# Kernel tuning notes

Measured on AMD Instinct MI355X. Metric: run time of the kernel, lower is better.

The kernel has to match this reference:

```python
import jax, jax.numpy as jnp
import numpy as np

DECAY = 0.1  # decay_rate from init

def setup_inputs() -> dict:
    key = jax.random.key(0)
    ks = jax.random.split(key, 6)
    B, S, D, H = 64, 512, 256, 512
    x = jax.random.normal(ks[0], (B, S, D), dtype=jnp.float32)
    # layer 0: Linear(D+H, 4H); layer 1: Linear(H+H, 4H). Stored as [in, out].
    W0 = jax.random.normal(ks[1], (D + H, 4 * H), dtype=jnp.float32) * (1.0 / np.sqrt(D + H))
    b0 = jnp.zeros((4 * H,), dtype=jnp.float32)
    W1 = jax.random.normal(ks[2], (H + H, 4 * H), dtype=jnp.float32) * (1.0 / np.sqrt(H + H))
    b1 = jnp.zeros((4 * H,), dtype=jnp.float32)
    efw = jnp.zeros((1, 1, D), dtype=jnp.float32)  # nn.Parameter(torch.ones) would be ones; use small init via zeros->exp=1 equiv scale
    efw = jnp.ones((1, 1, D), dtype=jnp.float32)
    return {"x": x, "W0": W0, "b0": b0, "W1": W1, "b1": b1, "efw": efw}

def _cell(x_t, h_prev, c_prev, W, b):
    # combined: [B, in+H]; gates: [B, 4H] split into i,f,g,o along feature dim
    gates = jnp.concatenate([x_t, h_prev], axis=1) @ W + b
    i, f, g, o = jnp.split(gates, 4, axis=1)
    i = jax.nn.sigmoid(i)
    f = jax.nn.sigmoid(f + c_prev) * (1.0 - DECAY)  # custom decayed forget gate
    g = jnp.tanh(g)
    o = jax.nn.sigmoid(o)
    c_next = f * c_prev + i * g
    h_next = o * jnp.tanh(c_next)
    return h_next, c_next

def reference(x, W0, b0, W1, b1, efw):
    B, S, D = x.shape
    H = W0.shape[1] // 4
    x = x * jnp.exp(efw)  # elementwise feature weighting
    xs = jnp.transpose(x, (1, 0, 2))  # [S, B, D] for scan over time
    init = (jnp.zeros((B, H), x.dtype), jnp.zeros((B, H), x.dtype),
            jnp.zeros((B, H), x.dtype), jnp.zeros((B, H), x.dtype))

    def step(carry, x_t):
        h0, c0, h1, c1 = carry
        h0, c0 = _cell(x_t, h0, c0, W0, b0)
        h1, c1 = _cell(h0, h1, c1, W1, b1)
        return (h0, c0, h1, c1), h1

    _, ys = jax.lax.scan(step, init, xs)  # ys: [S, B, H]
    return jnp.transpose(ys, (1, 0, 2))  # [B, S, H]
```

## Files before the change

### kernel.cpp

```cpp
#include <hip/hip_runtime.h>
#include <math.h>

#define B_   64
#define S_   512
#define D_   256
#define H_   512
#define G4   2048
#define K0   768
#define K1   1024
#define NWG  256
#define NAH  128
#define NTHR 256
#define BH   32768
#define NROT 4

#define OFF_GF   32
#define OFF_SCL  192
#define OFF_FLG  512
#define OFF_EPO  4608
#define OFF_TKT  4736
#define OFF_ACN  4864
#define OFF_RLS  4992
#define OFF_XCN  5120
#define OFF_H0   5248
#define OFF_H1   (OFF_H0 + 2*BH)
#define OFF_C0   (OFF_H1 + 2*BH)
#define OFF_C1   (OFF_C0 + BH)
#define OFF_ZEND (OFF_C1 + BH)
#define OFF_XBUF OFF_ZEND
#define XBUF_SZ  (8 * NROT * 2 * BH)
#define OFF_END  (OFF_XBUF + XBUF_SZ)

typedef __attribute__((ext_vector_type(4))) float f32x4;
typedef __attribute__((ext_vector_type(8))) short s16x8;

__device__ __forceinline__ float sigm(float v){ return 1.0f/(1.0f+expf(-v)); }
__device__ __forceinline__ unsigned short f2bf(float f){
  unsigned u = __builtin_bit_cast(unsigned, f);
  return (unsigned short)((u + 0x7FFFu + ((u>>16)&1u)) >> 16);
}
__device__ __forceinline__ float bf2f(unsigned short s){
  return __builtin_bit_cast(float, ((unsigned)s) << 16);
}
__device__ __forceinline__ void split8(const float* v, s16x8& h, s16x8& l){
#pragma unroll
  for (int e = 0; e < 8; ++e){
    unsigned short hs = f2bf(v[e]);
    h[e] = (short)hs;
    l[e] = (short)f2bf(v[e] - bf2f(hs));
  }
}

#define ALD(p)   __hip_atomic_load((p), __ATOMIC_RELAXED, __HIP_MEMORY_SCOPE_AGENT)
#define AST(p,v) __hip_atomic_store((p), (v), __ATOMIC_RELAXED, __HIP_MEMORY_SCOPE_AGENT)

__device__ __forceinline__ void xadd_noret(unsigned* p, unsigned v){
  asm volatile("global_atomic_add %0, %1, off\n\ts_waitcnt vmcnt(0)"
               :: "v"(p), "v"(v) : "memory");
}
__device__ __forceinline__ unsigned xadd_ret0(unsigned* p){
  unsigned r, z = 0u;
  asm volatile("global_atomic_add %0, %1, %2, off sc0\n\ts_waitcnt vmcnt(0)"
               : "=&v"(r) : "v"(p), "v"(z) : "memory");
  return r;
}
__device__ __forceinline__ void ld2x4_sc1(const float* p, f32x4& a, f32x4& b){
  asm volatile("global_load_dwordx4 %0, %2, off sc1\n\t"
               "global_load_dwordx4 %1, %2, off offset:16 sc1\n\t"
               "s_waitcnt vmcnt(0)"
               : "=&v"(a), "=&v"(b) : "v"(p) : "memory");
}

__global__ void lstm_init(const float* __restrict__ efw, float* __restrict__ ws){
  int stride = gridDim.x * blockDim.x;
  for (int j = blockIdx.x * blockDim.x + threadIdx.x; j < OFF_ZEND; j += stride){
    float v = 0.0f;
    if (j >= OFF_SCL && j < OFF_SCL + D_) v = expf(efw[j - OFF_SCL]);
    ws[j] = v;
  }
}

__launch_bounds__(NTHR, 1)
__global__ void lstm_persist(const float* __restrict__ x,
                             const float* __restrict__ W0,
                             const float* __restrict__ b0,
                             const float* __restrict__ W1,
                             const float* __restrict__ b1,
                             float* __restrict__ out,
                             float* __restrict__ ws)
{
  __shared__ short wfH[32*64*8];
  __shared__ short wfL[32*64*8];
  __shared__ short afH[16*64*8];
  __shared__ short afL[16*64*8];
  __shared__ float zB[64*17];
  __shared__ float scl[D_];
  __shared__ int   sslot;

  const int  wg  = blockIdx.x;
  const int  tid = threadIdx.x;
  const bool isA = (wg < NAH);
  const int  u0  = (isA ? wg : wg - NAH) * 4;
  const int  KI  = isA ? 24 : 32;
  const int  nch = isA ? 6 : 8;
  const int  lane = tid & 63;
  const int  wv_  = tid >> 6;

  float* h0 = ws + OFF_H0;
  float* h1 = ws + OFF_H1;
  float* cs = ws + (isA ? OFF_C0 : OFF_C1);
  short* XB = (short*)(ws + OFF_XBUF);
  unsigned* gf  = (unsigned*)ws + OFF_GF;
  unsigned* epo = (unsigned*)ws + OFF_EPO;
  unsigned* flg = (unsigned*)ws + OFF_FLG;
  unsigned* tkt = (unsigned*)ws + OFF_TKT;

  {
    const float* W = isA ? W0 : W1;
    for (int f = tid; f < KI*64; f += NTHR){
      int ki = f >> 6, ln = f & 63;
      int col = ln & 15, g = col >> 2, u2 = col & 3;
      int kb = ki*32 + ((ln >> 4) << 3);
      const float* wp = W + (size_t)kb * G4 + g * H_ + u0 + u2;
      s16x8 hh, ll;
#pragma unroll
      for (int e = 0; e < 8; ++e){
        float w = wp[(size_t)e * G4];
        unsigned short hs = f2bf(w);
        hh[e] = (short)hs;
        ll[e] = (short)f2bf(w - bf2f(hs));
      }
      *(s16x8*)&wfH[(size_t)f * 8] = hh;
      *(s16x8*)&wfL[(size_t)f * 8] = ll;
    }
  }
  for (int i = tid; i < D_; i += NTHR) scl[i] = ws[OFF_SCL + i];

  int xcc, slot, nx = 1;
  {
    xcc = (int)(__builtin_amdgcn_s_getreg(63508) & 7u);
    if (tid == 0)
      sslot = (int)__hip_atomic_fetch_add(tkt + (size_t)xcc*16, 1u,
                 __ATOMIC_RELAXED, __HIP_MEMORY_SCOPE_AGENT);
    __syncthreads();
    slot = sslot;
  }
  unsigned* acnt = (unsigned*)ws + OFF_ACN + (size_t)xcc*16;
  unsigned* rls  = (unsigned*)ws + OFF_RLS + (size_t)xcc*16;
  unsigned* xcnt = (unsigned*)ws + OFF_XCN + (size_t)xcc*16;

  auto gbar = [&](unsigned tgt){
    __syncthreads();
    if (tid == 0) AST(flg + (size_t)wg * 16, tgt);
    if (wg == 0 && tid < 64){
      for (;;){
        unsigned m0 = ALD(flg + (size_t)(tid       ) * 16);
        unsigned m1 = ALD(flg + (size_t)(tid +  64) * 16);
        unsigned m2 = ALD(flg + (size_t)(tid + 128) * 16);
        unsigned m3 = ALD(flg + (size_t)(tid + 192) * 16);
        if (__all(m0 >= tgt && m1 >= tgt && m2 >= tgt && m3 >= tgt)) break;
      }
      if (tid == 0){
#pragma unroll
        for (int kq = 0; kq < 8; ++kq) AST(epo + (size_t)kq * 16, tgt);
      }
    }
    if (tid < 64){
      while (ALD(epo + (size_t)(wg & 7) * 16) < tgt)
        __builtin_amdgcn_s_sleep(4);
    }
    __syncthreads();
  };

  auto hbar = [&](unsigned ev){
    __syncthreads();
    if (tid == 0){
      xadd_noret(acnt, 1u);
      if (slot == 0){
        const unsigned tgt = ev * (unsigned)nx;
        while (xadd_ret0(acnt) < tgt) __builtin_amdgcn_s_sleep(2);
      }
    }
    if (slot == 0 && tid < 64){
      if (tid == 0) AST(gf + (size_t)xcc * 16, ev);
      unsigned v = ev;
      for (;;){
        if (tid < 8) v = ALD(gf + (size_t)tid * 16);
        if (__all(v >= ev)) break;
        __builtin_amdgcn_s_sleep(2);
      }
      if (tid == 0) xadd_noret(rls, 1u);
    }
    if (tid == 0){
      while (xadd_ret0(rls) < ev) __builtin_amdgcn_s_sleep(4);
    }
    __syncthreads();
  };

  auto xbar = [&](unsigned ev){
    __syncthreads();
    if (tid == 0){
      xadd_noret(xcnt, 1u);
      const unsigned tgt = ev * (unsigned)nx;
      while (xadd_ret0(xcnt) < tgt) __builtin_amdgcn_s_sleep(4);
    }
    __syncthreads();
  };

  gbar(1u);
  nx = (int)ALD(tkt + (size_t)xcc * 16);

  auto stage_xcd = [&](int q, int rot){
    short* sbw = XB + ((size_t)(xcc * NROT + rot)) * (4 * BH);
    for (int s = slot; s < 32; s += nx){
      int off = s * 2048 + tid * 8;
      const float* gs = (off < BH) ? ws + OFF_H0 + (size_t)q * BH + off
                                   : ws + OFF_H1 + (size_t)q * BH + (off - BH);
      f32x4 a, b; ld2x4_sc1(gs, a, b);
      float v[8] = {a[0], a[1], a[2], a[3], b[0], b[1], b[2], b[3]};
      s16x8 hh, ll; split8(v, hh, ll);
      *(s16x8*)(sbw + off)          = hh;
      *(s16x8*)(sbw + 2*BH + off)   = ll;
    }
  };

  stage_xcd(1, 3);
  xbar(1u);

  const int row_r = tid & 63;
  const int uu    = tid >> 6;
  float bias[4];
  {
    const float* bv = isA ? b0 : b1;
#pragma unroll
    for (int g = 0; g < 4; ++g) bias[g] = bv[g * H_ + u0 + uu];
  }
  __syncthreads();

  const short* sb = nullptr;
  s16x8 rh[4], rl[4];
  const int r16 = tid & 15, ksl = (tid >> 4) & 3, kiq = tid >> 6;

  auto loadregs = [&](int c, int t){
    const int kk = c * 128 + kiq * 32 + ksl * 8;
#pragma unroll
    for (int j = 0; j < 4; ++j){
      const int row = 16 * j + r16;
      if (isA && kk < 256){
        const float* xp = x + ((size_t)row * S_ + t) * D_ + kk;
        float4 v0 = *(const float4*)xp;
        float4 v1 = *(const float4*)(xp + 4);
        float4 s0 = *(const float4*)&scl[kk];
        float4 s1 = *(const float4*)&scl[kk + 4];
        float v[8] = {v0.x*s0.x, v0.y*s0.y, v0.z*s0.z, v0.w*s0.w,
                      v1.x*s1.x, v1.y*s1.y, v1.z*s1.z, v1.w*s1.w};
        split8(v, rh[j], rl[j]);
      } else {
        const short* hp;
        if (isA)           hp = sb + (size_t)row * H_ + (kk - 256);
        else if (kk < 512) hp = sb + (size_t)row * H_ + kk;
        else               hp = sb + BH + (size_t)row * H_ + (kk - 512);
        rh[j] = *(const s16x8*)hp;
        rl[j] = *(const s16x8*)(hp + 2 * BH);
      }
    }
  };

  for (int r = 0; r <= S_; ++r){
    const bool act = isA ? (r < S_) : (r >= 1);
    if (act){
      const int t = isA ? r : r - 1;
      sb = XB + ((size_t)(xcc * NROT + ((r + 3) & 3))) * (4 * BH);
      f32x4 aHH = {0.f,0.f,0.f,0.f}, aHL = aHH, aLH = aHH;
      loadregs(0, t);

      for (int c = 0; c < nch; ++c){
        __syncthreads();
#pragma unroll
        for (int j = 0; j < 4; ++j){
          int fs = ((j * 4 + kiq) * 64 + lane) * 8;
          *(s16x8*)&afH[fs] = rh[j];
          *(s16x8*)&afL[fs] = rl[j];
        }
        if (c + 1 < nch) loadregs(c + 1, t);
        __syncthreads();
#pragma unroll
        for (int ki = 0; ki < 4; ++ki){
          int as  = ((wv_ * 4 + ki) * 64 + lane) * 8;
          int wsl = ((c * 4 + ki) * 64 + lane) * 8;
          s16x8 ah = *(const s16x8*)&afH[as];
          s16x8 al = *(const s16x8*)&afL[as];
          s16x8 wh = *(const s16x8*)&wfH[wsl];
          s16x8 wl = *(const s16x8*)&wfL[wsl];
          aHH = __builtin_amdgcn_mfma_f32_16x16x32_bf16(ah, wh, aHH, 0, 0, 0);
          aHL = __builtin_amdgcn_mfma_f32_16x16x32_bf16(ah, wl, aHL, 0, 0, 0);
          aLH = __builtin_amdgcn_mfma_f32_16x16x32_bf16(al, wh, aLH, 0, 0, 0);
        }
      }

      f32x4 accs = (aHH + aHL) + aLH;
#pragma unroll
      for (int reg = 0; reg < 4; ++reg){
        int row = 16 * wv_ + ((lane >> 4) << 2) + reg;
        zB[row * 17 + (lane & 15)] = accs[reg];
      }
      __syncthreads();
      {
        float z[4];
#pragma unroll
        for (int g = 0; g < 4; ++g) z[g] = zB[row_r * 17 + g * 4 + uu] + bias[g];
        const int ui = u0 + uu;
        float c_ = cs[(size_t)row_r * H_ + ui];
        float i_ = sigm(z[0]);
        float f_ = sigm(z[1] + c_) * 0.9f;
        float g_ = tanhf(z[2]);
        float o_ = sigm(z[3]);
        float cn = f_ * c_ + i_ * g_;
        float hn = o_ * tanhf(cn);
        cs[(size_t)row_r * H_ + ui] = cn;
        float* hw = (isA ? h0 : h1) + (size_t)(r & 1) * BH + (size_t)row_r * H_ + ui;
        AST(hw, hn);
        if (!isA) out[((size_t)row_r * S_ + t) * H_ + ui] = hn;
      }
    }

    if (r < S_){
      hbar((unsigned)(r + 1));
      stage_xcd(r & 1, r & 3);
      xbar((unsigned)(r + 2));
    }
  }
}

extern "C" void kernel_launch(void* const* d_in, const int* in_sizes, int n_in,
                              void* d_out, int out_size, void* d_ws, size_t ws_size,
                              hipStream_t stream){
  const float* x   = (const float*)d_in[0];
  const float* W0  = (const float*)d_in[1];
  const float* b0  = (const float*)d_in[2];
  const float* W1  = (const float*)d_in[3];
  const float* b1  = (const float*)d_in[4];
  const float* efw = (const float*)d_in[5];
  float* out = (float*)d_out;
  float* ws  = (float*)d_ws;

  if (ws_size < (size_t)OFF_END * sizeof(float)) return;

  lstm_init<<<256, 256, 0, stream>>>(efw, ws);
  lstm_persist<<<NWG, NTHR, 0, stream>>>(x, W0, b0, W1, b1, out, ws);
}
```

Measured before the change: 7.355 ms.

## Replace hierarchical h barrier with per-producer flags polled during staging

Removes the two-level hbar barrier (per-XCD counter, cross-XCD flag, release counter). Each workgroup now publishes a per-WG progress flag after writing its h values with an sc1 atomic swap. Staging threads poll only the flags of the producers whose columns they copy before loading and splitting them. The staging layout changes to row and 16-column tiles so each chunk depends on a small set of producers. This aims to shorten the per-step critical path of the grid-wide sync, at the cost of more polling traffic and reliance on memory-ordering semantics of the sc1 stores.

```diff
diff --git a/kernel.cpp b/kernel.cpp
--- a/kernel.cpp
+++ b/kernel.cpp
@@ -14,15 +14,13 @@
 #define BH   32768
 #define NROT 4
 
-#define OFF_GF   32
 #define OFF_SCL  192
 #define OFF_FLG  512
 #define OFF_EPO  4608
 #define OFF_TKT  4736
-#define OFF_ACN  4864
-#define OFF_RLS  4992
 #define OFF_XCN  5120
-#define OFF_H0   5248
+#define OFF_PFL  5248
+#define OFF_H0   9344
 #define OFF_H1   (OFF_H0 + 2*BH)
 #define OFF_C0   (OFF_H1 + 2*BH)
 #define OFF_C1   (OFF_C0 + BH)
@@ -33,6 +31,7 @@
 
 typedef __attribute__((ext_vector_type(4))) float f32x4;
 typedef __attribute__((ext_vector_type(8))) short s16x8;
+typedef __attribute__((ext_vector_type(4))) short s16x4;
 
 __device__ __forceinline__ float sigm(float v){ return 1.0f/(1.0f+expf(-v)); }
 __device__ __forceinline__ unsigned short f2bf(float f){
@@ -45,6 +44,14 @@
 __device__ __forceinline__ void split8(const float* v, s16x8& h, s16x8& l){
 #pragma unroll
   for (int e = 0; e < 8; ++e){
+    unsigned short hs = f2bf(v[e]);
+    h[e] = (short)hs;
+    l[e] = (short)f2bf(v[e] - bf2f(hs));
+  }
+}
+__device__ __forceinline__ void split4(const f32x4& v, s16x4& h, s16x4& l){
+#pragma unroll
+  for (int e = 0; e < 4; ++e){
     unsigned short hs = f2bf(v[e]);
     h[e] = (short)hs;
     l[e] = (short)f2bf(v[e] - bf2f(hs));
@@ -64,11 +71,17 @@
                : "=&v"(r) : "v"(p), "v"(z) : "memory");
   return r;
 }
-__device__ __forceinline__ void ld2x4_sc1(const float* p, f32x4& a, f32x4& b){
+__device__ __forceinline__ void hpub_sc1(float* p, float v){
+  unsigned b = __builtin_bit_cast(unsigned, v);
+  asm volatile("global_atomic_swap %0, %1, off sc1\n\ts_waitcnt vmcnt(0)"
+               :: "v"(p), "v"(b) : "memory");
+}
+__device__ __forceinline__ void ld_pair_sc1(const float* p0, const float* p1,
+                                            f32x4& a, f32x4& b){
   asm volatile("global_load_dwordx4 %0, %2, off sc1\n\t"
-               "global_load_dwordx4 %1, %2, off offset:16 sc1\n\t"
+               "global_load_dwordx4 %1, %3, off sc1\n\t"
                "s_waitcnt vmcnt(0)"
-               : "=&v"(a), "=&v"(b) : "v"(p) : "memory");
+               : "=&v"(a), "=&v"(b) : "v"(p0), "v"(p1) : "memory");
 }
 
 __global__ void lstm_init(const float* __restrict__ efw, float* __restrict__ ws){
@@ -110,10 +123,10 @@
   float* h1 = ws + OFF_H1;
   float* cs = ws + (isA ? OFF_C0 : OFF_C1);
   short* XB = (short*)(ws + OFF_XBUF);
-  unsigned* gf  = (unsigned*)ws + OFF_GF;
   unsigned* epo = (unsigned*)ws + OFF_EPO;
   unsigned* flg = (unsigned*)ws + OFF_FLG;
   unsigned* tkt = (unsigned*)ws + OFF_TKT;
+  unsigned* pfl = (unsigned*)ws + OFF_PFL;
 
   {
     const float* W = isA ? W0 : W1;
@@ -145,8 +158,6 @@
     __syncthreads();
     slot = sslot;
   }
-  unsigned* acnt = (unsigned*)ws + OFF_ACN + (size_t)xcc*16;
-  unsigned* rls  = (unsigned*)ws + OFF_RLS + (size_t)xcc*16;
   unsigned* xcnt = (unsigned*)ws + OFF_XCN + (size_t)xcc*16;
 
   auto gbar = [&](unsigned tgt){
@@ -172,37 +183,12 @@
     __syncthreads();
   };
 
-  auto hbar = [&](unsigned ev){
-    __syncthreads();
-    if (tid == 0){
-      xadd_noret(acnt, 1u);
-      if (slot == 0){
-        const unsigned tgt = ev * (unsigned)nx;
-        while (xadd_ret0(acnt) < tgt) __builtin_amdgcn_s_sleep(2);
-      }
-    }
-    if (slot == 0 && tid < 64){
-      if (tid == 0) AST(gf + (size_t)xcc * 16, ev);
-      unsigned v = ev;
-      for (;;){
-        if (tid < 8) v = ALD(gf + (size_t)tid * 16);
-        if (__all(v >= ev)) break;
-        __builtin_amdgcn_s_sleep(2);
-      }
-      if (tid == 0) xadd_noret(rls, 1u);
-    }
-    if (tid == 0){
-      while (xadd_ret0(rls) < ev) __builtin_amdgcn_s_sleep(4);
-    }
-    __syncthreads();
-  };
-
   auto xbar = [&](unsigned ev){
     __syncthreads();
     if (tid == 0){
       xadd_noret(xcnt, 1u);
       const unsigned tgt = ev * (unsigned)nx;
-      while (xadd_ret0(xcnt) < tgt) __builtin_amdgcn_s_sleep(4);
+      while (xadd_ret0(xcnt) < tgt) __builtin_amdgcn_s_sleep(2);
     }
     __syncthreads();
   };
@@ -210,21 +196,33 @@
   gbar(1u);
   nx = (int)ALD(tkt + (size_t)xcc * 16);
 
-  auto stage_xcd = [&](int q, int rot){
-    short* sbw = XB + ((size_t)(xcc * NROT + rot)) * (4 * BH);
-    for (int s = slot; s < 32; s += nx){
-      int off = s * 2048 + tid * 8;
-      const float* gs = (off < BH) ? ws + OFF_H0 + (size_t)q * BH + off
-                                   : ws + OFF_H1 + (size_t)q * BH + (off - BH);
-      f32x4 a, b; ld2x4_sc1(gs, a, b);
-      float v[8] = {a[0], a[1], a[2], a[3], b[0], b[1], b[2], b[3]};
-      s16x8 hh, ll; split8(v, hh, ll);
-      *(s16x8*)(sbw + off)          = hh;
-      *(s16x8*)(sbw + 2*BH + off)   = ll;
+  const int srow = tid >> 2, sc4 = (tid & 3) << 2;
+  auto stage_round = [&](int q, int rot, unsigned tag){
+    short* sbw = XB + ((size_t)(xcc * NROT + rot)) * (4 * (size_t)BH);
+    for (int g = slot; g < 32; g += nx){
+      int fidx = (lane < 4) ? (4*g + lane)
+               : (lane < 8 ? 128 + 4*g + (lane - 4) : -1);
+      unsigned v = tag;
+      for (;;){
+        if (fidx >= 0) v = ALD(pfl + (size_t)fidx * 16);
+        if (__all(v >= tag)) break;
+        __builtin_amdgcn_s_sleep(1);
+      }
+      const int col = 16*g + sc4;
+      const float* g0 = ws + OFF_H0 + (size_t)q * BH + (size_t)srow * H_ + col;
+      const float* g1 = ws + OFF_H1 + (size_t)q * BH + (size_t)srow * H_ + col;
+      f32x4 a, b; ld_pair_sc1(g0, g1, a, b);
+      s16x4 h0h, h0l, h1h, h1l;
+      split4(a, h0h, h0l); split4(b, h1h, h1l);
+      size_t o = (size_t)srow * H_ + col;
+      *(s16x4*)(sbw + o)                  = h0h;
+      *(s16x4*)(sbw + (size_t)BH + o)     = h1h;
+      *(s16x4*)(sbw + 2*(size_t)BH + o)   = h0l;
+      *(s16x4*)(sbw + 3*(size_t)BH + o)   = h1l;
     }
   };
 
-  stage_xcd(1, 3);
+  stage_round(1, 3, 0u);
   xbar(1u);
 
   const int row_r = tid & 63;
@@ -270,7 +268,7 @@
     const bool act = isA ? (r < S_) : (r >= 1);
     if (act){
       const int t = isA ? r : r - 1;
-      sb = XB + ((size_t)(xcc * NROT + ((r + 3) & 3))) * (4 * BH);
+      sb = XB + ((size_t)(xcc * NROT + ((r + 3) & 3))) * (4 * (size_t)BH);
       f32x4 aHH = {0.f,0.f,0.f,0.f}, aHL = aHH, aLH = aHH;
       loadregs(0, t);
 
@@ -318,15 +316,16 @@
         float cn = f_ * c_ + i_ * g_;
         float hn = o_ * tanhf(cn);
         cs[(size_t)row_r * H_ + ui] = cn;
+        if (!isA) out[((size_t)row_r * S_ + t) * H_ + ui] = hn;
         float* hw = (isA ? h0 : h1) + (size_t)(r & 1) * BH + (size_t)row_r * H_ + ui;
-        AST(hw, hn);
-        if (!isA) out[((size_t)row_r * S_ + t) * H_ + ui] = hn;
+        hpub_sc1(hw, hn);
       }
     }
 
     if (r < S_){
-      hbar((unsigned)(r + 1));
-      stage_xcd(r & 1, r & 3);
+      __syncthreads();
+      if (tid == 0) AST(pfl + (size_t)wg * 16, (unsigned)(r + 2));
+      stage_round(r & 1, r & 3, (unsigned)(r + 2));
       xbar((unsigned)(r + 2));
     }
   }
```

Result: faster. 6.918 ms (-5.9%).
